# Optimization experiments

Measured on AMD Instinct MI355X. Metric: run time of the kernel, lower is better.

The kernel has to match this reference:

```python
import jax, jax.numpy as jnp
import numpy as np

# Config constants (mirror ENNModelWithSparsityControl config)
NUM_LAYERS = 4
NUM_NEURONS = 131072
NUM_STATES = 32
DECAY_RATE = 0.9
RECENCY_FACTOR = 0.7
BUFFER_SIZE = 8
IMPORTANCE_THRESHOLD = 0.05
COMPRESSED_DIM = 16
SPARSITY_THRESHOLD = 0.01
LOW_POWER_K = 8
BATCH = 4


def setup_inputs() -> dict:
    key = jax.random.key(0)
    k = jax.random.split(key, 6)
    x = jax.random.normal(k[0], (BATCH, NUM_NEURONS, NUM_STATES), dtype=jnp.float32)
    neuron_states = jax.random.normal(k[1], (NUM_NEURONS, NUM_STATES), dtype=jnp.float32)
    # StateAutoEncoder params: encoder Linear(num_states->compressed_dim), decoder Linear(compressed_dim->num_states)
    Wenc = jax.random.normal(k[2], (COMPRESSED_DIM, NUM_STATES), dtype=jnp.float32) / np.sqrt(NUM_STATES)
    benc = jax.random.normal(k[3], (COMPRESSED_DIM,), dtype=jnp.float32) * 0.1
    Wdec = jax.random.normal(k[4], (NUM_STATES, COMPRESSED_DIM), dtype=jnp.float32) / np.sqrt(COMPRESSED_DIM)
    bdec = jax.random.normal(k[5], (NUM_STATES,), dtype=jnp.float32) * 0.1
    return {"x": x, "neuron_states": neuron_states, "Wenc": Wenc, "benc": benc, "Wdec": Wdec, "bdec": bdec}


def reference(x, neuron_states, Wenc, benc, Wdec, bdec):
    """Vectorized ENN forward: all per-neuron loops fused into array ops.

    Returns (x_out, final_neuron_states). The original forward returns x only,
    but neuron_states carries all of the kernel-relevant work, so we expose it.
    """
    N, S = neuron_states.shape
    B = BUFFER_SIZE
    states = neuron_states
    buffer = jnp.zeros((N, B, S), dtype=states.dtype)  # slot B-1 = newest
    slot = jnp.arange(B)
    ages = (B - 1 - slot).astype(states.dtype)  # age 0 = newest entry

    for layer in range(NUM_LAYERS):
        # dynamic_sparsity_control: zero out sub-threshold states
        states = jnp.where(jnp.abs(states) >= SPARSITY_THRESHOLD, states, 0.0)
        # state_decay
        states = states * DECAY_RATE
        # process_neuron_layer: per-neuron nonlinearity over [batch, N, S]
        x = jnp.tanh(x)
        # ShortTermBuffer.add_to_buffer (ring shift, append newest)
        buffer = jnp.concatenate([buffer[:, 1:], states[:, None, :]], axis=1)
        # temporal_proximity_scaling over valid recent activations
        count = min(layer + 1, B)  # static per layer
        valid = (slot >= B - count).astype(states.dtype)
        w = (RECENCY_FACTOR ** ages) * valid  # [B]
        states = jnp.einsum('b,nbs->ns', w, buffer) / w.sum()
        # advanced_state_collapse: autoencoder reconstruct + importance gate
        h = jax.nn.relu(states @ Wenc.T + benc)          # [N, compressed]
        rec = h @ Wdec.T + bdec                           # [N, S]
        states = jnp.where(jnp.abs(rec) >= IMPORTANCE_THRESHOLD, rec, 0.0)
        # low_power_state_collapse: keep top_k magnitudes per neuron
        topv = jax.lax.top_k(jnp.abs(states), LOW_POWER_K)[0]  # [N, k]
        kth = topv[:, -1:]
        states = jnp.where(jnp.abs(states) >= kth, states, 0.0)
    return x, states
```

## Files before the change

### kernel.cpp

```cpp
#include <hip/hip_runtime.h>

constexpr int N_NEURONS  = 131072;
constexpr int X_ELEMS    = 4 * 131072 * 32;
constexpr int X4         = X_ELEMS / 4;
constexpr int STATES_OFF = X_ELEMS;

__device__ __forceinline__ float fast_tanh(float x) {
  float a = fabsf(x);
  float e = __expf(2.0f * a);
  float t = 1.0f - __fdividef(2.0f, e + 1.0f);
  return copysignf(t, x);
}


__device__ double g_wenc_t[32 * 16];
__device__ double g_wdec[32 * 16];
__device__ double g_benc[16];
__device__ double g_bdec[32];

__global__ __launch_bounds__(256) void convert_weights_kernel(
    const float* __restrict__ Wenc, const float* __restrict__ benc,
    const float* __restrict__ Wdec, const float* __restrict__ bdec) {
  const int t = threadIdx.x;
  #pragma unroll
  for (int i = t; i < 512; i += 256) {
    const int k = i >> 4, c = i & 15;
    g_wenc_t[i] = (double)Wenc[c * 32 + k];
    g_wdec[i]   = (double)Wdec[i];
  }
  if (t < 16)              g_benc[t]      = (double)benc[t];
  if (t >= 64 && t < 96)   g_bdec[t - 64] = (double)bdec[t - 64];
}

__global__ __launch_bounds__(512)
void enn_fused_kernel(const float* __restrict__ x,
                      const float* __restrict__ ns,
                      float* __restrict__ out) {
  __shared__ double s_lds[32][256];

  const int tid = threadIdx.x;

  if (tid < 256) {
    const int n = blockIdx.x * 256 + tid;

    const float4* src = reinterpret_cast<const float4*>(ns) + (size_t)n * 8;
    #pragma unroll
    for (int j = 0; j < 8; ++j) {
      float4 v = src[j];
      s_lds[4 * j + 0][tid] = (double)v.x;
      s_lds[4 * j + 1][tid] = (double)v.y;
      s_lds[4 * j + 2][tid] = (double)v.z;
      s_lds[4 * j + 3][tid] = (double)v.w;
    }

    double ws[32];
    #pragma unroll
    for (int i = 0; i < 32; ++i) ws[i] = 0.0;

    double nrm = 0.0;
    double thr = 0.01;
    double kth = 0.0;
    #pragma unroll 1
    for (int layer = 0; layer < 4; ++layer) {
      nrm = nrm * 0.7 + 1.0;
      const double inv = 1.0 / nrm;

      #pragma unroll
      for (int k = 0; k < 32; ++k) {
        double v = s_lds[k][tid];
        v = (fabs(v) >= thr) ? v : 0.0;
        ws[k] = ws[k] * 0.7 + v * 0.9;
      }

      double hd[16];
      #pragma unroll
      for (int c = 0; c < 16; ++c) hd[c] = 0.0;
      #pragma unroll
      for (int k = 0; k < 32; ++k) {
        double wk = ws[k];
        #pragma unroll
        for (int c = 0; c < 16; ++c)
          hd[c] = fma(wk, g_wenc_t[k * 16 + c], hd[c]);
      }
      #pragma unroll
      for (int c = 0; c < 16; ++c)
        hd[c] = fmax(fma(hd[c], inv, g_benc[c]), 0.0);

      double ta[8], tb[8];
      #pragma unroll
      for (int k = 0; k < 8; ++k) { ta[k] = 0.0; tb[k] = 0.0; }
      #pragma unroll
      for (int i = 0; i < 32; ++i) {
        double acc = g_bdec[i];
        #pragma unroll
        for (int c = 0; c < 16; ++c)
          acc = fma(hd[c], g_wdec[i * 16 + c], acc);
        double r = (fabs(acc) >= 0.05) ? acc : 0.0;
        s_lds[i][tid] = r;
        double v = fabs(r);
        if ((i & 1) == 0) {
          #pragma unroll
          for (int k = 0; k < 8; ++k) {
            double hi = fmax(ta[k], v);
            v = fmin(ta[k], v);
            ta[k] = hi;
          }
        } else {
          #pragma unroll
          for (int k = 0; k < 8; ++k) {
            double hi = fmax(tb[k], v);
            v = fmin(tb[k], v);
            tb[k] = hi;
          }
        }
      }
      double m0 = fmax(ta[0], tb[7]), m1 = fmax(ta[1], tb[6]);
      double m2 = fmax(ta[2], tb[5]), m3 = fmax(ta[3], tb[4]);
      double m4 = fmax(ta[4], tb[3]), m5 = fmax(ta[5], tb[2]);
      double m6 = fmax(ta[6], tb[1]), m7 = fmax(ta[7], tb[0]);
      kth = fmin(fmin(fmin(m0, m1), fmin(m2, m3)),
                 fmin(fmin(m4, m5), fmin(m6, m7)));
      thr = fmax(kth, 0.01);
    }

    float4* dst = reinterpret_cast<float4*>(out + STATES_OFF) + (size_t)n * 8;
    #pragma unroll
    for (int j = 0; j < 8; ++j) {
      float r[4];
      #pragma unroll
      for (int q = 0; q < 4; ++q) {
        double v = s_lds[4 * j + q][tid];
        r[q] = (float)((fabs(v) >= kth) ? v : 0.0);
      }
      dst[j] = make_float4(r[0], r[1], r[2], r[3]);
    }
  } else {
    const int xt = tid - 256;
    const float4* xb = reinterpret_cast<const float4*>(x);
    float4*       ob = reinterpret_cast<float4*>(out);
    const size_t base = (size_t)blockIdx.x * 8192 + xt;

    #pragma unroll 1
    for (int j = 0; j < 32; j += 4) {
      float4 v0 = xb[base + (size_t)(j + 0) * 256];
      float4 v1 = xb[base + (size_t)(j + 1) * 256];
      float4 v2 = xb[base + (size_t)(j + 2) * 256];
      float4 v3 = xb[base + (size_t)(j + 3) * 256];
      #pragma unroll
      for (int r = 0; r < 4; ++r) {
        v0.x = fast_tanh(v0.x); v0.y = fast_tanh(v0.y);
        v0.z = fast_tanh(v0.z); v0.w = fast_tanh(v0.w);
        v1.x = fast_tanh(v1.x); v1.y = fast_tanh(v1.y);
        v1.z = fast_tanh(v1.z); v1.w = fast_tanh(v1.w);
        v2.x = fast_tanh(v2.x); v2.y = fast_tanh(v2.y);
        v2.z = fast_tanh(v2.z); v2.w = fast_tanh(v2.w);
        v3.x = fast_tanh(v3.x); v3.y = fast_tanh(v3.y);
        v3.z = fast_tanh(v3.z); v3.w = fast_tanh(v3.w);
      }
      ob[base + (size_t)(j + 0) * 256] = v0;
      ob[base + (size_t)(j + 1) * 256] = v1;
      ob[base + (size_t)(j + 2) * 256] = v2;
      ob[base + (size_t)(j + 3) * 256] = v3;
    }
  }
}

extern "C" void kernel_launch(void* const* d_in, const int* in_sizes, int n_in,
                              void* d_out, int out_size, void* d_ws, size_t ws_size,
                              hipStream_t stream) {
  const float* x    = (const float*)d_in[0];
  const float* ns   = (const float*)d_in[1];
  const float* Wenc = (const float*)d_in[2];
  const float* benc = (const float*)d_in[3];
  const float* Wdec = (const float*)d_in[4];
  const float* bdec = (const float*)d_in[5];
  float* out = (float*)d_out;

  convert_weights_kernel<<<1, 256, 0, stream>>>(Wenc, benc, Wdec, bdec);
  enn_fused_kernel<<<N_NEURONS / 256, 512, 0, stream>>>(x, ns, out);
}
```

Before: 229.9 us.

## Carry encoder projection across layers and replace insertion top-k with sorting networks

Uses linearity of the encoder to keep a running 16-wide projected accumulator instead of the 32-wide weighted buffer, then applies decay and normalisation as one scale. This cuts register state and moves the 0.9 decay into the final scale. The per-neuron top-8 selection over 32 values now uses 8-element sorting networks with bitonic merges instead of serial insertion into two sorted lists. Together these aim to lower double-precision ALU work and register pressure in the compute-bound neuron path, at the cost of a slightly different floating-point summation order.

```diff
diff --git a/kernel.cpp b/kernel.cpp
--- a/kernel.cpp
+++ b/kernel.cpp
@@ -32,6 +32,32 @@
   if (t >= 64 && t < 96)   g_bdec[t - 64] = (double)bdec[t - 64];
 }
 
+__device__ __forceinline__ void ce(double& a, double& b) {
+  double hi = fmax(a, b);
+  b = fmin(a, b);
+  a = hi;
+}
+
+__device__ __forceinline__ void sortnet8_abs(double q[8]) {
+  #pragma unroll
+  for (int j = 0; j < 8; j += 2) {
+    double hi = fmax(fabs(q[j]), fabs(q[j + 1]));
+    double lo = fmin(fabs(q[j]), fabs(q[j + 1]));
+    q[j] = hi; q[j + 1] = lo;
+  }
+  ce(q[0], q[2]); ce(q[1], q[3]); ce(q[1], q[2]);
+  ce(q[4], q[6]); ce(q[5], q[7]); ce(q[5], q[6]);
+  ce(q[0], q[4]); ce(q[1], q[5]); ce(q[2], q[6]); ce(q[3], q[7]);
+  ce(q[2], q[4]); ce(q[3], q[5]);
+  ce(q[1], q[2]); ce(q[3], q[4]); ce(q[5], q[6]);
+}
+
+__device__ __forceinline__ void bitonic8(double m[8]) {
+  ce(m[0], m[4]); ce(m[1], m[5]); ce(m[2], m[6]); ce(m[3], m[7]);
+  ce(m[0], m[2]); ce(m[1], m[3]); ce(m[4], m[6]); ce(m[5], m[7]);
+  ce(m[0], m[1]); ce(m[2], m[3]); ce(m[4], m[5]); ce(m[6], m[7]);
+}
+
 __global__ __launch_bounds__(512)
 void enn_fused_kernel(const float* __restrict__ x,
                       const float* __restrict__ ns,
@@ -53,9 +79,9 @@
       s_lds[4 * j + 3][tid] = (double)v.w;
     }
 
-    double ws[32];
+    double u[16];
     #pragma unroll
-    for (int i = 0; i < 32; ++i) ws[i] = 0.0;
+    for (int c = 0; c < 16; ++c) u[c] = 0.0;
 
     double nrm = 0.0;
     double thr = 0.01;
@@ -63,63 +89,54 @@
     #pragma unroll 1
     for (int layer = 0; layer < 4; ++layer) {
       nrm = nrm * 0.7 + 1.0;
-      const double inv = 1.0 / nrm;
+      const double inv9 = 0.9 / nrm;
 
+      #pragma unroll
+      for (int c = 0; c < 16; ++c) u[c] = u[c] * 0.7;
       #pragma unroll
       for (int k = 0; k < 32; ++k) {
         double v = s_lds[k][tid];
         v = (fabs(v) >= thr) ? v : 0.0;
-        ws[k] = ws[k] * 0.7 + v * 0.9;
+        #pragma unroll
+        for (int c = 0; c < 16; ++c)
+          u[c] = fma(v, g_wenc_t[k * 16 + c], u[c]);
       }
 
       double hd[16];
       #pragma unroll
-      for (int c = 0; c < 16; ++c) hd[c] = 0.0;
+      for (int c = 0; c < 16; ++c)
+        hd[c] = fmax(fma(u[c], inv9, g_benc[c]), 0.0);
+
+      double qa[8], qb[8], A[8], B[8];
       #pragma unroll
-      for (int k = 0; k < 32; ++k) {
-        double wk = ws[k];
+      for (int half = 0; half < 2; ++half) {
         #pragma unroll
-        for (int c = 0; c < 16; ++c)
-          hd[c] = fma(wk, g_wenc_t[k * 16 + c], hd[c]);
+        for (int g = 0; g < 2; ++g) {
+          double* q = g ? qb : qa;
+          const int base = half * 16 + g * 8;
+          #pragma unroll
+          for (int ii = 0; ii < 8; ++ii) {
+            const int i = base + ii;
+            double acc = g_bdec[i];
+            #pragma unroll
+            for (int c = 0; c < 16; ++c)
+              acc = fma(hd[c], g_wdec[i * 16 + c], acc);
+            double r = (fabs(acc) >= 0.05) ? acc : 0.0;
+            s_lds[i][tid] = r;
+            q[ii] = r;
+          }
+          if (g) sortnet8_abs(qb); else sortnet8_abs(qa);
+        }
+        double* T = half ? B : A;
+        #pragma unroll
+        for (int j = 0; j < 8; ++j) T[j] = fmax(qa[j], qb[7 - j]);
+        if (half) bitonic8(B); else bitonic8(A);
       }
+      double m[8];
       #pragma unroll
-      for (int c = 0; c < 16; ++c)
-        hd[c] = fmax(fma(hd[c], inv, g_benc[c]), 0.0);
-
-      double ta[8], tb[8];
-      #pragma unroll
-      for (int k = 0; k < 8; ++k) { ta[k] = 0.0; tb[k] = 0.0; }
-      #pragma unroll
-      for (int i = 0; i < 32; ++i) {
-        double acc = g_bdec[i];
-        #pragma unroll
-        for (int c = 0; c < 16; ++c)
-          acc = fma(hd[c], g_wdec[i * 16 + c], acc);
-        double r = (fabs(acc) >= 0.05) ? acc : 0.0;
-        s_lds[i][tid] = r;
-        double v = fabs(r);
-        if ((i & 1) == 0) {
-          #pragma unroll
-          for (int k = 0; k < 8; ++k) {
-            double hi = fmax(ta[k], v);
-            v = fmin(ta[k], v);
-            ta[k] = hi;
-          }
-        } else {
-          #pragma unroll
-          for (int k = 0; k < 8; ++k) {
-            double hi = fmax(tb[k], v);
-            v = fmin(tb[k], v);
-            tb[k] = hi;
-          }
-        }
-      }
-      double m0 = fmax(ta[0], tb[7]), m1 = fmax(ta[1], tb[6]);
-      double m2 = fmax(ta[2], tb[5]), m3 = fmax(ta[3], tb[4]);
-      double m4 = fmax(ta[4], tb[3]), m5 = fmax(ta[5], tb[2]);
-      double m6 = fmax(ta[6], tb[1]), m7 = fmax(ta[7], tb[0]);
-      kth = fmin(fmin(fmin(m0, m1), fmin(m2, m3)),
-                 fmin(fmin(m4, m5), fmin(m6, m7)));
+      for (int j = 0; j < 8; ++j) m[j] = fmax(A[j], B[7 - j]);
+      kth = fmin(fmin(fmin(m[0], m[1]), fmin(m[2], m[3])),
+                 fmin(fmin(m[4], m[5]), fmin(m[6], m[7])));
       thr = fmax(kth, 0.01);
     }
 
```

Result: faster. 193.9 us (-15.7%).
